# Kernel optimization log

Measured on AMD Instinct MI355X. Metric: run time of the kernel, lower is better.

## Reference

```python
import jax, jax.numpy as jnp
import numpy as np

# MoE config (matches init_kwargs)
E = 32      # num_experts
K = 4       # num_experts_per_tok (top_k)
H = 1024    # hidden_size
I = 512     # moe_intermediate_size (shared expert uses I * num_shared_experts = I)
B, S = 2, 2048
T = B * S
C = 1024
ROUTED_SCALE = 1.0


def _silu_and_mul(gu):
    g, u = jnp.split(gu, 2, axis=-1)
    return jax.nn.silu(g) * u


def setup_inputs() -> dict:
    key = jax.random.key(0)
    ks = jax.random.split(key, 6)
    s = 0.02
    return {
        "hidden_states": jax.random.normal(ks[0], (B, S, H), jnp.float32),
        "gate_w": jax.random.normal(ks[1], (E, H), jnp.float32) * s,
        "w_gate_up": jax.random.normal(ks[2], (E, H, 2 * I), jnp.float32) * s,
        "w_down": jax.random.normal(ks[3], (E, I, H), jnp.float32) * s,
        "shared_w_gate_up": jax.random.normal(ks[4], (H, 2 * I), jnp.float32) * s,
        "shared_w_down": jax.random.normal(ks[5], (I, H), jnp.float32) * s,
    }


def reference(hidden_states, gate_w, w_gate_up, w_down, shared_w_gate_up, shared_w_down):
    b, s, h = hidden_states.shape
    x = hidden_states.reshape(-1, h)                      # [T, H]
    t = x.shape[0]

    # --- router: gate linear -> softmax -> top-k -> renormalize ---
    logits = x @ gate_w.T                                 # [T, E]
    probs = jax.nn.softmax(logits, axis=-1)
    topk_w, topk_idx = jax.lax.top_k(probs, K)            # [T, K]
    topk_w = topk_w / jnp.sum(topk_w, axis=-1, keepdims=True)  # norm_topk_prob
    topk_w = topk_w * ROUTED_SCALE

    # --- dispatch: sort (token, slot) assignments by expert, scatter into capacity buffer ---
    e_flat = topk_idx.reshape(-1)                         # [T*K]
    w_flat = topk_w.reshape(-1)
    t_flat = jnp.repeat(jnp.arange(t), K)
    order = jnp.argsort(e_flat)                           # stable sort by expert id
    e_s, w_s, t_s = e_flat[order], w_flat[order], t_flat[order]
    counts = jax.ops.segment_sum(jnp.ones_like(e_s), e_s, num_segments=E)
    starts = jnp.cumsum(counts) - counts                  # exclusive prefix sum
    pos = jnp.arange(t * K) - starts[e_s]                 # position within expert group
    slot = jnp.minimum(pos, C)                            # overflow -> trash slot C
    buf = jnp.zeros((E, C + 1, h), x.dtype).at[e_s, slot].set(x[t_s])

    # --- grouped expert MLP (silu-gated) ---
    gu = jnp.einsum('ech,ehi->eci', buf[:, :C], w_gate_up)        # [E, C, 2I]
    expert_out = jnp.einsum('eci,eih->ech', _silu_and_mul(gu), w_down)  # [E, C, H]
    expert_out = jnp.pad(expert_out, ((0, 0), (0, 1), (0, 0)))    # trash slot reads zero

    # --- combine: gather back, weight, scatter-add per token ---
    gate = jnp.where(pos < C, w_s, 0.0)[:, None]
    routed = jnp.zeros_like(x).at[t_s].add(expert_out[e_s, slot] * gate)

    # --- shared expert MLP ---
    shared = _silu_and_mul(x @ shared_w_gate_up) @ shared_w_down

    return (routed + shared).reshape(b, s, h)
```

## Files before the change

kernel.cpp:

```cpp
#include <hip/hip_runtime.h>
#include <cstdint>
#include <cstddef>

#define NEXP   32
#define TOPK   4
#define HD     1024
#define ID     512
#define TT     4096
#define CAP    1024
#define SHARED_BASE (NEXP*CAP)
#define NSLOT  (NEXP*CAP + TT)
#define MAXTILES 320

#define KSPLIT 16
#define KCH    64
#define KSUB   16

typedef __attribute__((ext_vector_type(4))) float f32x4;
typedef __bf16 bf16x8 __attribute__((ext_vector_type(8)));

__device__ __forceinline__ unsigned short f2bf(float f) {
    union { float f; unsigned int u; } v; v.f = f;
    unsigned int u = v.u;
    u = (u + 0x7FFFu + ((u >> 16) & 1u)) >> 16;
    return (unsigned short)u;
}
__device__ __forceinline__ float bf2f(unsigned short s) {
    union { unsigned int u; float f; } v; v.u = ((unsigned int)s) << 16;
    return v.f;
}

#define GLOAD_LDS16(g, l)                                                     \
    __builtin_amdgcn_global_load_lds(                                         \
        (__attribute__((address_space(1))) void*)(g),                         \
        (__attribute__((address_space(3))) void*)(l), 16, 0, 0)

__global__ __launch_bounds__(256)
void k_prep(const float* __restrict__ wgu, const float* __restrict__ sgu,
            const float* __restrict__ wdn, const float* __restrict__ sdn,
            unsigned short* __restrict__ wgup_t, unsigned short* __restrict__ wdn_t,
            const float* __restrict__ x, const float* __restrict__ gw,
            float* __restrict__ part, unsigned short* __restrict__ xb) {
    __shared__ __align__(16) char smem[18944];
    const int z = blockIdx.z;
    const int tid = threadIdx.x;

    if (z < 66) {
        const float* src; const float* srcS; unsigned short* dst; int K, N, zz;
        if (z < 33) { src = wgu; srcS = sgu; dst = wgup_t; K = 1024; N = 1024; zz = z; }
        else {
            if (blockIdx.y >= 8) return;
            src = wdn; srcS = sdn; dst = wdn_t; K = 512; N = 1024; zz = z - 33;
        }
        float (*ld)[65] = reinterpret_cast<float(*)[65]>(smem);
        const size_t esz = (size_t)K * N;
        const float* s = (zz < NEXP) ? src + (size_t)zz * esz : srcS;
        dst += (size_t)zz * esz;
        const int n0 = blockIdx.x * 64, k0 = blockIdx.y * 64;
        const int c4 = (tid & 15) * 4;
        const int rbase = tid >> 4;
#pragma unroll
        for (int p = 0; p < 4; p++) {
            int row = rbase + p * 16;
            float4 v = *(const float4*)(s + (size_t)(k0 + row) * N + n0 + c4);
            ld[row][c4 + 0] = v.x; ld[row][c4 + 1] = v.y;
            ld[row][c4 + 2] = v.z; ld[row][c4 + 3] = v.w;
        }
        __syncthreads();
        const int n  = tid >> 2;
        const int ks = (tid & 3) * 16;
        unsigned short tmp[16];
#pragma unroll
        for (int i = 0; i < 16; i++) tmp[i] = f2bf(ld[ks + i][n]);
        uint4 a, b;
        a.x = tmp[0] | (tmp[1] << 16);  a.y = tmp[2] | (tmp[3] << 16);
        a.z = tmp[4] | (tmp[5] << 16);  a.w = tmp[6] | (tmp[7] << 16);
        b.x = tmp[8] | (tmp[9] << 16);  b.y = tmp[10] | (tmp[11] << 16);
        b.z = tmp[12] | (tmp[13] << 16); b.w = tmp[14] | (tmp[15] << 16);
        unsigned short* op = dst + (size_t)(n0 + n) * K + k0 + ks;
        *(uint4*)op = a;
        *(uint4*)(op + 8) = b;
        return;
    }

    float (*xsT)[260] = reinterpret_cast<float(*)[260]>(smem);
    float (*gsT)[36]  = reinterpret_cast<float(*)[36]>(smem + KSUB * 260 * 4);
    const int lane = tid & 63, wv = tid >> 6;
    const int tg = lane >> 2, eg = lane & 3;
    const int t0 = blockIdx.x * 256;
    const int kbase = blockIdx.y * KCH;
    const int tbase = wv * 64 + tg * 4;
    const int ebase = eg * 8;

    float acc[4][8];
#pragma unroll
    for (int j = 0; j < 4; j++)
#pragma unroll
        for (int i = 0; i < 8; i++) acc[j][i] = 0.f;

    for (int ks = 0; ks < KCH; ks += KSUB) {
        const int k0 = kbase + ks;
        if (ks > 0) __syncthreads();
#pragma unroll
        for (int p = 0; p < 4; p++) {
            int vid = p * 256 + tid;
            int t = vid >> 2, kq = (vid & 3) * 4;
            float4 v = *(const float4*)(x + (size_t)(t0 + t) * HD + k0 + kq);
            xsT[kq + 0][t] = v.x; xsT[kq + 1][t] = v.y;
            xsT[kq + 2][t] = v.z; xsT[kq + 3][t] = v.w;
            ushort4 o;
            o.x = f2bf(v.x); o.y = f2bf(v.y); o.z = f2bf(v.z); o.w = f2bf(v.w);
            *(ushort4*)(xb + (size_t)(t0 + t) * HD + k0 + kq) = o;
        }
#pragma unroll
        for (int p = 0; p < 2; p++) {
            int vid = p * 256 + tid;
            int e = vid >> 4, k = vid & 15;
            gsT[k][e] = gw[(size_t)e * HD + k0 + k];
        }
        __syncthreads();
#pragma unroll 4
        for (int k = 0; k < KSUB; k++) {
            float4 xv = *(const float4*)&xsT[k][tbase];
            float4 g0 = *(const float4*)&gsT[k][ebase];
            float4 g1 = *(const float4*)&gsT[k][ebase + 4];
            float xa[4] = {xv.x, xv.y, xv.z, xv.w};
#pragma unroll
            for (int j = 0; j < 4; j++) {
                acc[j][0] += xa[j] * g0.x; acc[j][1] += xa[j] * g0.y;
                acc[j][2] += xa[j] * g0.z; acc[j][3] += xa[j] * g0.w;
                acc[j][4] += xa[j] * g1.x; acc[j][5] += xa[j] * g1.y;
                acc[j][6] += xa[j] * g1.z; acc[j][7] += xa[j] * g1.w;
            }
        }
    }
    const size_t base = ((size_t)blockIdx.y * TT + (t0 + tbase)) * 32 + ebase;
#pragma unroll
    for (int j = 0; j < 4; j++) {
        float4 w0, w1;
        w0.x = acc[j][0]; w0.y = acc[j][1]; w0.z = acc[j][2]; w0.w = acc[j][3];
        w1.x = acc[j][4]; w1.y = acc[j][5]; w1.z = acc[j][6]; w1.w = acc[j][7];
        *(float4*)(part + base + (size_t)j * 32) = w0;
        *(float4*)(part + base + (size_t)j * 32 + 4) = w1;
    }
}

__global__ __launch_bounds__(256)
void k_topk(const float* __restrict__ part,
            int* __restrict__ choice, float* __restrict__ cw,
            int* __restrict__ tok, float* __restrict__ wgt) {
    const int lane = threadIdx.x & 63, wv = threadIdx.x >> 6;
    const int t = blockIdx.x * 4 + wv;
    const int e = lane & 31;
    const int sbase = (lane >> 5) * 8;
    float v = 0.f;
#pragma unroll
    for (int s = 0; s < 8; s++)
        v += part[((size_t)(sbase + s) * TT + t) * 32 + e];
    v += __shfl_xor(v, 32);
    float sc = (lane < 32) ? v : -INFINITY;

    float lv[TOPK]; int le[TOPK];
#pragma unroll
    for (int r = 0; r < TOPK; r++) {
        float m = sc;
#pragma unroll
        for (int d = 1; d < 64; d <<= 1) m = fmaxf(m, __shfl_xor(m, d));
        unsigned long long ball = __ballot(sc == m);
        int widx = __ffsll(ball) - 1;
        lv[r] = m; le[r] = widx;
        if (lane == widx) sc = -INFINITY;
    }
    if (lane == 0) {
        float wv4[TOPK], wsum = 0.f;
#pragma unroll
        for (int r = 0; r < TOPK; r++) { wv4[r] = __expf(lv[r] - lv[0]); wsum += wv4[r]; }
#pragma unroll
        for (int r = 0; r < TOPK; r++) {
            choice[t * TOPK + r] = le[r];
            cw[t * TOPK + r] = wv4[r] / wsum;
        }
        tok[SHARED_BASE + t] = t;
        wgt[SHARED_BASE + t] = 1.0f;
    }
}

__global__ __launch_bounds__(1024)
void k_assign(const int* __restrict__ choice, const float* __restrict__ cw,
              int* __restrict__ cnt, int* __restrict__ tok,
              float* __restrict__ wgt, int* __restrict__ smap) {
    const int e = blockIdx.x;
    const int tid = threadIdx.x, lane = tid & 63, wv = tid >> 6;
    __shared__ int wtot[16];
    int running = 0;
    for (int it = 0; it < TT / 1024; it++) {
        const int t = it * 1024 + tid;
        const int4   c4 = *(const int4*)(choice + t * 4);
        const float4 w4 = *(const float4*)(cw + t * 4);
        unsigned m = (unsigned)(c4.x == e) | ((unsigned)(c4.y == e) << 1)
                   | ((unsigned)(c4.z == e) << 2) | ((unsigned)(c4.w == e) << 3);
        int mc = __popc(m);
        int pre = mc;
#pragma unroll
        for (int d = 1; d < 64; d <<= 1) {
            int up = __shfl_up(pre, d);
            if (lane >= d) pre += up;
        }
        if (lane == 63) wtot[wv] = pre;
        const int wpre = pre - mc;
        __syncthreads();
        int woff = 0, tot = 0;
#pragma unroll
        for (int w = 0; w < 16; w++) { int c = wtot[w]; tot += c; if (w < wv) woff += c; }
        int base = running + woff + wpre;
        running += tot;
        __syncthreads();
        if (m) {
            const float wa[4] = {w4.x, w4.y, w4.z, w4.w};
            int k = 0;
#pragma unroll
            for (int r = 0; r < 4; r++) {
                if (m & (1u << r)) {
                    int pos = base + k;
                    int i = t * 4 + r;
                    if (pos < CAP) {
                        int slot = e * CAP + pos;
                        tok[slot] = t;
                        wgt[slot] = wa[r];
                        smap[i] = slot;
                    } else {
                        smap[i] = -1;
                    }
                    k++;
                }
            }
        }
    }
    if (tid == 0) cnt[e] = min(running, CAP);
}

template <int KD, bool GATHER, bool SILU>
__global__ __launch_bounds__(256)
void k_moe_gemm(const unsigned short* __restrict__ Ab,
                const unsigned short* __restrict__ Bt,
                unsigned short* __restrict__ Cout,
                const int* __restrict__ tok,
                const int* __restrict__ cnt) {
    const int tid  = threadIdx.x;
    const int lane = tid & 63;
    const int wv   = tid >> 6;

    int c_l = (lane < NEXP) ? min(cnt[lane], CAP) : ((lane == NEXP) ? TT : 0);
    int nt_l = (c_l + 127) >> 7;
    int pre = nt_l;
#pragma unroll
    for (int d = 1; d < 64; d <<= 1) {
        int up = __shfl_up(pre, d);
        if (lane >= d) pre += up;
    }
    const int ntl = __shfl(pre, 63);
    const int chunk = (ntl + 7) >> 3;
    const int c_xcd = blockIdx.x;
    const int qy = blockIdx.y;
    if ((qy >> 3) >= chunk) return;
    const int j = c_xcd * chunk + (qy >> 3);
    if (j >= ntl) return;
    const int nt = qy & 7;
    const int start_l = pre - nt_l;
    const bool mine = (j >= start_l) && (j < start_l + nt_l);
    const unsigned long long bl = __ballot(mine);
    const int e_lane = __ffsll((long long)bl) - 1;
    const int e  = e_lane;
    const int mt = j - __shfl(start_l, e_lane);
    const int cE = __shfl(c_l, e_lane);

    const int slotbase = (e < NEXP) ? e * CAP : SHARED_BASE;
    const int m0 = mt * 128;
    const int rowsv = min(128, cE - m0);

    const unsigned short* Bte = Bt + (size_t)e * (1024 * KD);

    __shared__ unsigned short As[3][128 * 32];
    __shared__ unsigned short Bs[3][128 * 32];

    const int rr  = lane >> 2;
    const int seg = (lane & 3) ^ ((lane >> 3) & 3);
    const int r0 = wv * 32 + rr;
    const int r1 = r0 + 16;

    int ga0 = m0 + r0, ga1 = m0 + r1;
    int ra0, ra1;
    if (GATHER) {
        ra0 = (ga0 < cE) ? tok[slotbase + ga0] : 0;
        ra1 = (ga1 < cE) ? tok[slotbase + ga1] : 0;
    } else {
        ra0 = slotbase + ga0;
        ra1 = slotbase + ga1;
    }
    const unsigned short* ap0 = Ab + (size_t)ra0 * KD + seg * 8;
    const unsigned short* ap1 = Ab + (size_t)ra1 * KD + seg * 8;

    int br0, br1;
    if (SILU) {
        int in0 = r0 & 63, in1 = r1 & 63;
        int c0 = nt * 64 + (r0 >> 6) * 32 + (in0 & 31);
        int c1 = nt * 64 + (r1 >> 6) * 32 + (in1 & 31);
        br0 = (in0 < 32) ? c0 : 512 + c0;
        br1 = (in1 < 32) ? c1 : 512 + c1;
    } else {
        br0 = nt * 128 + r0;
        br1 = nt * 128 + r1;
    }
    const unsigned short* bp0 = Bte + (size_t)br0 * KD + seg * 8;
    const unsigned short* bp1 = Bte + (size_t)br1 * KD + seg * 8;

    const int aoff0 = (wv * 32) * 32, aoff1 = (wv * 32 + 16) * 32;

    f32x4 acc[4][4];
#pragma unroll
    for (int i = 0; i < 4; i++)
#pragma unroll
        for (int j2 = 0; j2 < 4; j2++) acc[i][j2] = (f32x4)(0.0f);

    const int mrow = lane & 15;
    const int quad = lane >> 4;
    const int wm = wv >> 1, wn = wv & 1;
    const int sw = (quad ^ ((mrow >> 1) & 3)) * 8;

    const int aRdOff = (wm * 64 + mrow) * 32 + sw;
    const int bRdOff = (wn * 64 + mrow) * 32 + sw;

    GLOAD_LDS16(ap0, As[0] + aoff0);
    GLOAD_LDS16(ap1, As[0] + aoff1);
    GLOAD_LDS16(bp0, Bs[0] + aoff0);
    GLOAD_LDS16(bp1, Bs[0] + aoff1);
    GLOAD_LDS16(ap0 + 32, As[1] + aoff0);
    GLOAD_LDS16(ap1 + 32, As[1] + aoff1);
    GLOAD_LDS16(bp0 + 32, Bs[1] + aoff0);
    GLOAD_LDS16(bp1 + 32, Bs[1] + aoff1);

    int p = 0;
    for (int k0 = 0; k0 < KD; k0 += 32) {
        if (k0 + 32 < KD) {
            asm volatile("s_waitcnt vmcnt(4) lgkmcnt(0)" ::: "memory");
        } else {
            asm volatile("s_waitcnt vmcnt(0) lgkmcnt(0)" ::: "memory");
        }
        __builtin_amdgcn_s_barrier();
        asm volatile("" ::: "memory");

        const int kn = k0 + 64;
        if (kn < KD) {
            int pw = p + 2; if (pw >= 3) pw -= 3;
            GLOAD_LDS16(ap0 + kn, As[pw] + aoff0);
            GLOAD_LDS16(ap1 + kn, As[pw] + aoff1);
            GLOAD_LDS16(bp0 + kn, Bs[pw] + aoff0);
            GLOAD_LDS16(bp1 + kn, Bs[pw] + aoff1);
        }

        bf16x8 af[4], bf[4];
#pragma unroll
        for (int i = 0; i < 4; i++) {
            af[i] = *(const bf16x8*)(As[p] + aRdOff + i * 16 * 32);
            bf[i] = *(const bf16x8*)(Bs[p] + bRdOff + i * 16 * 32);
        }
#pragma unroll
        for (int mi = 0; mi < 4; mi++)
#pragma unroll
            for (int nj = 0; nj < 4; nj++)
                acc[mi][nj] = __builtin_amdgcn_mfma_f32_16x16x32_bf16(
                    af[mi], bf[nj], acc[mi][nj], 0, 0, 0);
        p++; if (p >= 3) p = 0;
    }

    if (SILU) {
#pragma unroll
        for (int mi = 0; mi < 4; mi++)
#pragma unroll
            for (int nj = 0; nj < 2; nj++) {
                f32x4 g = acc[mi][nj];
                f32x4 u = acc[mi][nj + 2];
#pragma unroll
                for (int r = 0; r < 4; r++) {
                    int rloc = wm * 64 + mi * 16 + quad * 4 + r;
                    if (rloc < rowsv) {
                        float gv = g[r], uv = u[r];
                        float a = (gv / (1.f + __expf(-gv))) * uv;
                        int c = nt * 64 + wn * 32 + nj * 16 + mrow;
                        Cout[(size_t)(slotbase + m0 + rloc) * ID + c] = f2bf(a);
                    }
                }
            }
    } else {
#pragma unroll
        for (int mi = 0; mi < 4; mi++)
#pragma unroll
            for (int nj = 0; nj < 4; nj++) {
                f32x4 v = acc[mi][nj];
#pragma unroll
                for (int r = 0; r < 4; r++) {
                    int rloc = wm * 64 + mi * 16 + quad * 4 + r;
                    if (rloc < rowsv) {
                        int c = nt * 128 + wn * 64 + nj * 16 + mrow;
                        Cout[(size_t)(slotbase + m0 + rloc) * HD + c] = f2bf(v[r]);
                    }
                }
            }
    }
}

__global__ __launch_bounds__(256)
void k_combine(const unsigned short* __restrict__ eout,
               const int* __restrict__ smap,
               const float* __restrict__ wgt,
               float* __restrict__ out) {
    const int t = blockIdx.x;
    const int h0 = threadIdx.x * 4;
    ushort4 q = *(const ushort4*)(eout + (size_t)(SHARED_BASE + t) * HD + h0);
    float a0 = bf2f(q.x), a1 = bf2f(q.y), a2 = bf2f(q.z), a3 = bf2f(q.w);
#pragma unroll
    for (int r = 0; r < TOPK; r++) {
        int slot = smap[t * TOPK + r];
        if (slot >= 0) {
            float w = wgt[slot];
            ushort4 e4 = *(const ushort4*)(eout + (size_t)slot * HD + h0);
            a0 += w * bf2f(e4.x); a1 += w * bf2f(e4.y);
            a2 += w * bf2f(e4.z); a3 += w * bf2f(e4.w);
        }
    }
    float4 o; o.x = a0; o.y = a1; o.z = a2; o.w = a3;
    *(float4*)(out + (size_t)t * HD + h0) = o;
}

extern "C" void kernel_launch(void* const* d_in, const int* in_sizes, int n_in,
                              void* d_out, int out_size, void* d_ws, size_t ws_size,
                              hipStream_t stream) {
    const float* x   = (const float*)d_in[0];
    const float* gw  = (const float*)d_in[1];
    const float* wgu = (const float*)d_in[2];
    const float* wdn = (const float*)d_in[3];
    const float* sgu = (const float*)d_in[4];
    const float* sdn = (const float*)d_in[5];
    float* out = (float*)d_out;

    char* w = (char*)d_ws;
    size_t off = 0;
    int* cnt = (int*)(w + off);                       off += 256;
    unsigned short* xb     = (unsigned short*)(w + off); off += (size_t)TT * HD * 2;
    unsigned short* wgup_t = (unsigned short*)(w + off); off += (size_t)33 * 1024 * 1024 * 2;
    unsigned short* wdn_t  = (unsigned short*)(w + off); off += (size_t)33 * 1024 * 512 * 2;
    unsigned short* act    = (unsigned short*)(w + off); off += (size_t)NSLOT * ID * 2;
    int*   tok    = (int*)(w + off);   off += (size_t)NSLOT * 4;
    float* wgt    = (float*)(w + off); off += (size_t)NSLOT * 4;
    int*   smap   = (int*)(w + off);   off += (size_t)TT * TOPK * 4;
    int*   choice = (int*)(w + off);   off += (size_t)TT * TOPK * 4;
    float* cw     = (float*)(w + off); off += (size_t)TT * TOPK * 4;

    float* part = (float*)act;
    unsigned short* eout = xb;

    k_prep<<<dim3(16, 16, 67), 256, 0, stream>>>(wgu, sgu, wdn, sdn,
                                                 wgup_t, wdn_t, x, gw, part, xb);
    k_topk<<<TT / 4, 256, 0, stream>>>(part, choice, cw, tok, wgt);
    k_assign<<<NEXP, 1024, 0, stream>>>(choice, cw, cnt, tok, wgt, smap);

    k_moe_gemm<1024, true, true><<<dim3(8, MAXTILES), 256, 0, stream>>>(xb, wgup_t, act, tok, cnt);
    k_moe_gemm<512, false, false><<<dim3(8, MAXTILES), 256, 0, stream>>>(act, wdn_t, eout, tok, cnt);

    k_combine<<<TT, 256, 0, stream>>>(eout, smap, wgt, out);
}
```

Measured before the change: 417.5 us.

## Pipeline weight transpose-convert with async LDS loads and fewer router K-splits

```diff
diff --git a/kernel.cpp b/kernel.cpp
--- a/kernel.cpp
+++ b/kernel.cpp
@@ -12,8 +12,8 @@
 #define NSLOT  (NEXP*CAP + TT)
 #define MAXTILES 320
 
-#define KSPLIT 16
-#define KCH    64
+#define KSPLIT 4
+#define KCH    256
 #define KSUB   16
 
 typedef __attribute__((ext_vector_type(4))) float f32x4;
@@ -41,46 +41,74 @@
             unsigned short* __restrict__ wgup_t, unsigned short* __restrict__ wdn_t,
             const float* __restrict__ x, const float* __restrict__ gw,
             float* __restrict__ part, unsigned short* __restrict__ xb) {
-    __shared__ __align__(16) char smem[18944];
+    __shared__ __align__(16) char smem[49152];
     const int z = blockIdx.z;
     const int tid = threadIdx.x;
 
     if (z < 66) {
-        const float* src; const float* srcS; unsigned short* dst; int K, N, zz;
-        if (z < 33) { src = wgu; srcS = sgu; dst = wgup_t; K = 1024; N = 1024; zz = z; }
+        const float* src; const float* srcS; unsigned short* dst; int K, zz;
+        if (z < 33) { src = wgu; srcS = sgu; dst = wgup_t; K = 1024; zz = z; }
         else {
-            if (blockIdx.y >= 8) return;
-            src = wdn; srcS = sdn; dst = wdn_t; K = 512; N = 1024; zz = z - 33;
-        }
-        float (*ld)[65] = reinterpret_cast<float(*)[65]>(smem);
+            if (blockIdx.y >= 2) return;
+            src = wdn; srcS = sdn; dst = wdn_t; K = 512; zz = z - 33;
+        }
+        const int N = 1024;
+        float* ring = reinterpret_cast<float*>(smem);
         const size_t esz = (size_t)K * N;
         const float* s = (zz < NEXP) ? src + (size_t)zz * esz : srcS;
         dst += (size_t)zz * esz;
-        const int n0 = blockIdx.x * 64, k0 = blockIdx.y * 64;
-        const int c4 = (tid & 15) * 4;
-        const int rbase = tid >> 4;
-#pragma unroll
-        for (int p = 0; p < 4; p++) {
-            int row = rbase + p * 16;
-            float4 v = *(const float4*)(s + (size_t)(k0 + row) * N + n0 + c4);
-            ld[row][c4 + 0] = v.x; ld[row][c4 + 1] = v.y;
-            ld[row][c4 + 2] = v.z; ld[row][c4 + 3] = v.w;
-        }
-        __syncthreads();
+        const int n0 = blockIdx.x * 64;
+        const int kb = blockIdx.y * 256;
+        const int lane = tid & 63, wv2 = tid >> 6;
+        const int sig_w = (0x5140 >> (wv2 * 4)) & 7;
+        const int pp = (lane & 15) ^ sig_w;
+
+#define TSTAGE(ss, b)                                                         \
+        {                                                                     \
+            _Pragma("unroll")                                                 \
+            for (int q = 0; q < 4; q++) {                                     \
+                int rl = wv2 * 16 + q * 4 + (lane >> 4);                      \
+                const float* gp = s + (size_t)(kb + (ss) * 64 + rl) * N       \
+                                    + n0 + pp * 4;                            \
+                GLOAD_LDS16(gp, ring + (b) * 4096 + (wv2 * 16 + q * 4) * 64); \
+            }                                                                 \
+        }
         const int n  = tid >> 2;
         const int ks = (tid & 3) * 16;
-        unsigned short tmp[16];
-#pragma unroll
-        for (int i = 0; i < 16; i++) tmp[i] = f2bf(ld[ks + i][n]);
-        uint4 a, b;
-        a.x = tmp[0] | (tmp[1] << 16);  a.y = tmp[2] | (tmp[3] << 16);
-        a.z = tmp[4] | (tmp[5] << 16);  a.w = tmp[6] | (tmp[7] << 16);
-        b.x = tmp[8] | (tmp[9] << 16);  b.y = tmp[10] | (tmp[11] << 16);
-        b.z = tmp[12] | (tmp[13] << 16); b.w = tmp[14] | (tmp[15] << 16);
-        unsigned short* op = dst + (size_t)(n0 + n) * K + k0 + ks;
-        *(uint4*)op = a;
-        *(uint4*)(op + 8) = b;
+        const int sig_r = (0x5140 >> ((tid & 3) * 4)) & 7;
+        const int slot = (n >> 2) ^ sig_r;
+#define TPROC(ss, b)                                                          \
+        {                                                                     \
+            const float* rbp = ring + (b) * 4096 + ks * 64 + slot * 4 + (n & 3); \
+            unsigned short tmp[16];                                           \
+            _Pragma("unroll")                                                 \
+            for (int i = 0; i < 16; i++) tmp[i] = f2bf(rbp[i * 64]);          \
+            uint4 a, bq;                                                      \
+            a.x = tmp[0] | (tmp[1] << 16);  a.y = tmp[2] | (tmp[3] << 16);    \
+            a.z = tmp[4] | (tmp[5] << 16);  a.w = tmp[6] | (tmp[7] << 16);    \
+            bq.x = tmp[8] | (tmp[9] << 16);  bq.y = tmp[10] | (tmp[11] << 16);\
+            bq.z = tmp[12] | (tmp[13] << 16); bq.w = tmp[14] | (tmp[15] << 16);\
+            unsigned short* op = dst + (size_t)(n0 + n) * K + kb + (ss) * 64 + ks; \
+            *(uint4*)op = a;                                                  \
+            *(uint4*)(op + 8) = bq;                                           \
+        }
+
+        TSTAGE(0, 0); TSTAGE(1, 1);
+        asm volatile("s_waitcnt vmcnt(4)" ::: "memory");
+        __builtin_amdgcn_s_barrier();
+        TSTAGE(2, 2); TPROC(0, 0);
+        asm volatile("s_waitcnt vmcnt(6)" ::: "memory");
+        __builtin_amdgcn_s_barrier();
+        TSTAGE(3, 0); TPROC(1, 1);
+        asm volatile("s_waitcnt vmcnt(8)" ::: "memory");
+        __builtin_amdgcn_s_barrier();
+        TPROC(2, 2);
+        asm volatile("s_waitcnt vmcnt(4)" ::: "memory");
+        __builtin_amdgcn_s_barrier();
+        TPROC(3, 0);
         return;
+#undef TSTAGE
+#undef TPROC
     }
 
     float (*xsT)[260] = reinterpret_cast<float(*)[260]>(smem);
@@ -152,10 +180,10 @@
     const int lane = threadIdx.x & 63, wv = threadIdx.x >> 6;
     const int t = blockIdx.x * 4 + wv;
     const int e = lane & 31;
-    const int sbase = (lane >> 5) * 8;
+    const int sbase = (lane >> 5) * 2;
     float v = 0.f;
 #pragma unroll
-    for (int s = 0; s < 8; s++)
+    for (int s = 0; s < 2; s++)
         v += part[((size_t)(sbase + s) * TT + t) * 32 + e];
     v += __shfl_xor(v, 32);
     float sc = (lane < 32) ? v : -INFINITY;
@@ -459,8 +487,8 @@
     float* part = (float*)act;
     unsigned short* eout = xb;
 
-    k_prep<<<dim3(16, 16, 67), 256, 0, stream>>>(wgu, sgu, wdn, sdn,
-                                                 wgup_t, wdn_t, x, gw, part, xb);
+    k_prep<<<dim3(16, 4, 67), 256, 0, stream>>>(wgu, sgu, wdn, sdn,
+                                                wgup_t, wdn_t, x, gw, part, xb);
     k_topk<<<TT / 4, 256, 0, stream>>>(part, choice, cw, tok, wgt);
     k_assign<<<NEXP, 1024, 0, stream>>>(choice, cw, cnt, tok, wgt, smap);
 
```

Measured after the change: 429.0 us. 1.03x slower.

## Double-buffer weight transpose in prep kernel, processing four K-chunks per block

Applied to the files above, without the earlier changes.

```diff
diff --git a/kernel.cpp b/kernel.cpp
--- a/kernel.cpp
+++ b/kernel.cpp
@@ -12,8 +12,8 @@
 #define NSLOT  (NEXP*CAP + TT)
 #define MAXTILES 320
 
-#define KSPLIT 16
-#define KCH    64
+#define KSPLIT 4
+#define KCH    256
 #define KSUB   16
 
 typedef __attribute__((ext_vector_type(4))) float f32x4;
@@ -41,45 +41,70 @@
             unsigned short* __restrict__ wgup_t, unsigned short* __restrict__ wdn_t,
             const float* __restrict__ x, const float* __restrict__ gw,
             float* __restrict__ part, unsigned short* __restrict__ xb) {
-    __shared__ __align__(16) char smem[18944];
+    __shared__ __align__(16) char smem[33280];
     const int z = blockIdx.z;
     const int tid = threadIdx.x;
 
     if (z < 66) {
-        const float* src; const float* srcS; unsigned short* dst; int K, N, zz;
-        if (z < 33) { src = wgu; srcS = sgu; dst = wgup_t; K = 1024; N = 1024; zz = z; }
+        const float* src; const float* srcS; unsigned short* dst; int K, zz;
+        if (z < 33) { src = wgu; srcS = sgu; dst = wgup_t; K = 1024; zz = z; }
         else {
-            if (blockIdx.y >= 8) return;
-            src = wdn; srcS = sdn; dst = wdn_t; K = 512; N = 1024; zz = z - 33;
-        }
-        float (*ld)[65] = reinterpret_cast<float(*)[65]>(smem);
+            if (blockIdx.y >= 2) return;
+            src = wdn; srcS = sdn; dst = wdn_t; K = 512; zz = z - 33;
+        }
+        const int N = 1024;
+        float (*ld)[64][65] = reinterpret_cast<float(*)[64][65]>(smem);
         const size_t esz = (size_t)K * N;
         const float* s = (zz < NEXP) ? src + (size_t)zz * esz : srcS;
         dst += (size_t)zz * esz;
-        const int n0 = blockIdx.x * 64, k0 = blockIdx.y * 64;
+        const int n0 = blockIdx.x * 64;
+        const int kb = blockIdx.y * 256;
         const int c4 = (tid & 15) * 4;
         const int rbase = tid >> 4;
+        const int n  = tid >> 2;
+        const int ks = (tid & 3) * 16;
+
+        float4 rg[4];
+#pragma unroll
+        for (int p = 0; p < 4; p++)
+            rg[p] = *(const float4*)(s + (size_t)(kb + rbase + p * 16) * N + n0 + c4);
 #pragma unroll
         for (int p = 0; p < 4; p++) {
             int row = rbase + p * 16;
-            float4 v = *(const float4*)(s + (size_t)(k0 + row) * N + n0 + c4);
-            ld[row][c4 + 0] = v.x; ld[row][c4 + 1] = v.y;
-            ld[row][c4 + 2] = v.z; ld[row][c4 + 3] = v.w;
-        }
-        __syncthreads();
-        const int n  = tid >> 2;
-        const int ks = (tid & 3) * 16;
-        unsigned short tmp[16];
-#pragma unroll
-        for (int i = 0; i < 16; i++) tmp[i] = f2bf(ld[ks + i][n]);
-        uint4 a, b;
-        a.x = tmp[0] | (tmp[1] << 16);  a.y = tmp[2] | (tmp[3] << 16);
-        a.z = tmp[4] | (tmp[5] << 16);  a.w = tmp[6] | (tmp[7] << 16);
-        b.x = tmp[8] | (tmp[9] << 16);  b.y = tmp[10] | (tmp[11] << 16);
-        b.z = tmp[12] | (tmp[13] << 16); b.w = tmp[14] | (tmp[15] << 16);
-        unsigned short* op = dst + (size_t)(n0 + n) * K + k0 + ks;
-        *(uint4*)op = a;
-        *(uint4*)(op + 8) = b;
+            ld[0][row][c4 + 0] = rg[p].x; ld[0][row][c4 + 1] = rg[p].y;
+            ld[0][row][c4 + 2] = rg[p].z; ld[0][row][c4 + 3] = rg[p].w;
+        }
+
+#pragma unroll
+        for (int sIt = 0; sIt < 4; sIt++) {
+            const int cur = sIt & 1;
+            float4 rg2[4];
+            if (sIt < 3) {
+#pragma unroll
+                for (int p = 0; p < 4; p++)
+                    rg2[p] = *(const float4*)(s + (size_t)(kb + (sIt + 1) * 64 + rbase + p * 16) * N + n0 + c4);
+            }
+            __syncthreads();
+            unsigned short tmp[16];
+#pragma unroll
+            for (int i = 0; i < 16; i++) tmp[i] = f2bf(ld[cur][ks + i][n]);
+            uint4 a, bq;
+            a.x = tmp[0] | (tmp[1] << 16);  a.y = tmp[2] | (tmp[3] << 16);
+            a.z = tmp[4] | (tmp[5] << 16);  a.w = tmp[6] | (tmp[7] << 16);
+            bq.x = tmp[8] | (tmp[9] << 16);  bq.y = tmp[10] | (tmp[11] << 16);
+            bq.z = tmp[12] | (tmp[13] << 16); bq.w = tmp[14] | (tmp[15] << 16);
+            unsigned short* op = dst + (size_t)(n0 + n) * K + kb + sIt * 64 + ks;
+            *(uint4*)op = a;
+            *(uint4*)(op + 8) = bq;
+            if (sIt < 3) {
+#pragma unroll
+                for (int p = 0; p < 4; p++) {
+                    int row = rbase + p * 16;
+                    ld[cur ^ 1][row][c4 + 0] = rg2[p].x; ld[cur ^ 1][row][c4 + 1] = rg2[p].y;
+                    ld[cur ^ 1][row][c4 + 2] = rg2[p].z; ld[cur ^ 1][row][c4 + 3] = rg2[p].w;
+                }
+            }
+        }
         return;
     }
 
@@ -152,10 +177,10 @@
     const int lane = threadIdx.x & 63, wv = threadIdx.x >> 6;
     const int t = blockIdx.x * 4 + wv;
     const int e = lane & 31;
-    const int sbase = (lane >> 5) * 8;
+    const int sbase = (lane >> 5) * 2;
     float v = 0.f;
 #pragma unroll
-    for (int s = 0; s < 8; s++)
+    for (int s = 0; s < 2; s++)
         v += part[((size_t)(sbase + s) * TT + t) * 32 + e];
     v += __shfl_xor(v, 32);
     float sc = (lane < 32) ? v : -INFINITY;
@@ -459,8 +484,8 @@
     float* part = (float*)act;
     unsigned short* eout = xb;
 
-    k_prep<<<dim3(16, 16, 67), 256, 0, stream>>>(wgu, sgu, wdn, sdn,
-                                                 wgup_t, wdn_t, x, gw, part, xb);
+    k_prep<<<dim3(16, 4, 67), 256, 0, stream>>>(wgu, sgu, wdn, sdn,
+                                                wgup_t, wdn_t, x, gw, part, xb);
     k_topk<<<TT / 4, 256, 0, stream>>>(part, choice, cw, tok, wgt);
     k_assign<<<NEXP, 1024, 0, stream>>>(choice, cw, cnt, tok, wgt, smap);
 
```

Measured after the change: 427.7 us. 1.02x slower.

## Drop weight transpose in prep; transpose B tiles in-register into LDS inside GEMM

Applied to the files above, without the earlier changes.

```diff
diff --git a/kernel.cpp b/kernel.cpp
--- a/kernel.cpp
+++ b/kernel.cpp
@@ -38,7 +38,7 @@
 __global__ __launch_bounds__(256)
 void k_prep(const float* __restrict__ wgu, const float* __restrict__ sgu,
             const float* __restrict__ wdn, const float* __restrict__ sdn,
-            unsigned short* __restrict__ wgup_t, unsigned short* __restrict__ wdn_t,
+            unsigned short* __restrict__ wgup_b, unsigned short* __restrict__ wdn_b,
             const float* __restrict__ x, const float* __restrict__ gw,
             float* __restrict__ part, unsigned short* __restrict__ xb) {
     __shared__ __align__(16) char smem[18944];
@@ -46,40 +46,26 @@
     const int tid = threadIdx.x;
 
     if (z < 66) {
-        const float* src; const float* srcS; unsigned short* dst; int K, N, zz;
-        if (z < 33) { src = wgu; srcS = sgu; dst = wgup_t; K = 1024; N = 1024; zz = z; }
-        else {
-            if (blockIdx.y >= 8) return;
-            src = wdn; srcS = sdn; dst = wdn_t; K = 512; N = 1024; zz = z - 33;
-        }
-        float (*ld)[65] = reinterpret_cast<float(*)[65]>(smem);
-        const size_t esz = (size_t)K * N;
-        const float* s = (zz < NEXP) ? src + (size_t)zz * esz : srcS;
-        dst += (size_t)zz * esz;
-        const int n0 = blockIdx.x * 64, k0 = blockIdx.y * 64;
-        const int c4 = (tid & 15) * 4;
-        const int rbase = tid >> 4;
-#pragma unroll
-        for (int p = 0; p < 4; p++) {
-            int row = rbase + p * 16;
-            float4 v = *(const float4*)(s + (size_t)(k0 + row) * N + n0 + c4);
-            ld[row][c4 + 0] = v.x; ld[row][c4 + 1] = v.y;
-            ld[row][c4 + 2] = v.z; ld[row][c4 + 3] = v.w;
-        }
-        __syncthreads();
-        const int n  = tid >> 2;
-        const int ks = (tid & 3) * 16;
-        unsigned short tmp[16];
-#pragma unroll
-        for (int i = 0; i < 16; i++) tmp[i] = f2bf(ld[ks + i][n]);
-        uint4 a, b;
-        a.x = tmp[0] | (tmp[1] << 16);  a.y = tmp[2] | (tmp[3] << 16);
-        a.z = tmp[4] | (tmp[5] << 16);  a.w = tmp[6] | (tmp[7] << 16);
-        b.x = tmp[8] | (tmp[9] << 16);  b.y = tmp[10] | (tmp[11] << 16);
-        b.z = tmp[12] | (tmp[13] << 16); b.w = tmp[14] | (tmp[15] << 16);
-        unsigned short* op = dst + (size_t)(n0 + n) * K + k0 + ks;
-        *(uint4*)op = a;
-        *(uint4*)(op + 8) = b;
+        const float* s; unsigned short* d;
+        const int lb = blockIdx.y * 16 + blockIdx.x;
+        if (z < 33) {
+            s = (z < NEXP) ? wgu + (size_t)z * (1024 * 1024) : sgu;
+            d = wgup_b + (size_t)z * (1024 * 1024);
+        } else {
+            if (lb >= 128) return;
+            int zz = z - 33;
+            s = (zz < NEXP) ? wdn + (size_t)zz * (512 * 1024) : sdn;
+            d = wdn_b + (size_t)zz * (512 * 1024);
+        }
+        const size_t base = (size_t)lb * 1024;
+#pragma unroll
+        for (int j = 0; j < 4; j++) {
+            size_t i = base + j * 256 + tid;
+            float4 v = ((const float4*)s)[i];
+            ushort4 o;
+            o.x = f2bf(v.x); o.y = f2bf(v.y); o.z = f2bf(v.z); o.w = f2bf(v.w);
+            ((ushort4*)d)[i] = o;
+        }
         return;
     }
 
@@ -278,13 +264,13 @@
     const int m0 = mt * 128;
     const int rowsv = min(128, cE - m0);
 
-    const unsigned short* Bte = Bt + (size_t)e * (1024 * KD);
+    const unsigned short* Bte = Bt + (size_t)e * ((size_t)KD * 1024);
 
     __shared__ unsigned short As[3][128 * 32];
-    __shared__ unsigned short Bs[3][128 * 32];
-
-    const int rr  = lane >> 2;
-    const int seg = (lane & 3) ^ ((lane >> 3) & 3);
+    __shared__ unsigned short Bs[2][128 * 32];
+
+    const int rr   = lane >> 2;
+    const int segA = (lane & 3) ^ ((lane >> 4) & 3);
     const int r0 = wv * 32 + rr;
     const int r1 = r0 + 16;
 
@@ -297,24 +283,57 @@
         ra0 = slotbase + ga0;
         ra1 = slotbase + ga1;
     }
-    const unsigned short* ap0 = Ab + (size_t)ra0 * KD + seg * 8;
-    const unsigned short* ap1 = Ab + (size_t)ra1 * KD + seg * 8;
-
-    int br0, br1;
+    const unsigned short* ap0 = Ab + (size_t)ra0 * KD + segA * 8;
+    const unsigned short* ap1 = Ab + (size_t)ra1 * KD + segA * 8;
+    const int aoff0 = (wv * 32) * 32, aoff1 = (wv * 32 + 16) * 32;
+
+    const int hB = lane >> 5;
+    const int nw = lane & 31;
+    int rB[4], offB[4];
+    int bcol;
     if (SILU) {
-        int in0 = r0 & 63, in1 = r1 & 63;
-        int c0 = nt * 64 + (r0 >> 6) * 32 + (in0 & 31);
-        int c1 = nt * 64 + (r1 >> 6) * 32 + (in1 & 31);
-        br0 = (in0 < 32) ? c0 : 512 + c0;
-        br1 = (in1 < 32) ? c1 : 512 + c1;
+        const int sn0 = nw * 4;
+        const int side = sn0 >> 6;
+        const int jj0 = sn0 & 63;
+        bcol = (side ? 512 : 0) + nt * 64 + jj0;
+#pragma unroll
+        for (int q = 0; q < 4; q++) {
+            int jj = jj0 + q;
+            rB[q] = ((jj >> 5) << 6) + (side << 5) + (jj & 31);
+        }
     } else {
-        br0 = nt * 128 + r0;
-        br1 = nt * 128 + r1;
-    }
-    const unsigned short* bp0 = Bte + (size_t)br0 * KD + seg * 8;
-    const unsigned short* bp1 = Bte + (size_t)br1 * KD + seg * 8;
-
-    const int aoff0 = (wv * 32) * 32, aoff1 = (wv * 32 + 16) * 32;
+        bcol = nt * 128 + nw * 4;
+#pragma unroll
+        for (int q = 0; q < 4; q++) rB[q] = nw * 4 + q;
+    }
+#pragma unroll
+    for (int q = 0; q < 4; q++) {
+        int slot = wv ^ ((rB[q] >> 2) & 3);
+        offB[q] = rB[q] * 32 + slot * 8 + hB * 4;
+    }
+    const unsigned short* bp = Bte + (size_t)(wv * 8 + hB * 4) * 1024 + bcol;
+
+#define BLOAD(IT, R0, R1, R2, R3)                                             \
+    {                                                                         \
+        const unsigned short* bpk = bp + (size_t)(IT) * 32 * 1024;            \
+        R0 = *(const uint2*)(bpk);                                            \
+        R1 = *(const uint2*)(bpk + 1024);                                     \
+        R2 = *(const uint2*)(bpk + 2048);                                     \
+        R3 = *(const uint2*)(bpk + 3072);                                     \
+    }
+#define BPACK(BUF, R0, R1, R2, R3)                                            \
+    {                                                                         \
+        unsigned short* bw = &Bs[BUF][0];                                     \
+        _Pragma("unroll")                                                     \
+        for (int q = 0; q < 4; q++) {                                         \
+            unsigned e0 = ((q < 2 ? R0.x : R0.y) >> (16 * (q & 1))) & 0xffffu;\
+            unsigned e1 = ((q < 2 ? R1.x : R1.y) >> (16 * (q & 1))) & 0xffffu;\
+            unsigned e2 = ((q < 2 ? R2.x : R2.y) >> (16 * (q & 1))) & 0xffffu;\
+            unsigned e3 = ((q < 2 ? R3.x : R3.y) >> (16 * (q & 1))) & 0xffffu;\
+            uint2 wv2; wv2.x = e0 | (e1 << 16); wv2.y = e2 | (e3 << 16);      \
+            *(uint2*)(bw + offB[q]) = wv2;                                    \
+        }                                                                     \
+    }
 
     f32x4 acc[4][4];
 #pragma unroll
@@ -325,44 +344,44 @@
     const int mrow = lane & 15;
     const int quad = lane >> 4;
     const int wm = wv >> 1, wn = wv & 1;
-    const int sw = (quad ^ ((mrow >> 1) & 3)) * 8;
+    const int sw = (quad ^ ((mrow >> 2) & 3)) * 8;
 
     const int aRdOff = (wm * 64 + mrow) * 32 + sw;
     const int bRdOff = (wn * 64 + mrow) * 32 + sw;
 
+    uint2 rb0, rb1, rb2, rb3;
+    BLOAD(0, rb0, rb1, rb2, rb3);
+    __builtin_amdgcn_sched_barrier(0);
     GLOAD_LDS16(ap0, As[0] + aoff0);
     GLOAD_LDS16(ap1, As[0] + aoff1);
-    GLOAD_LDS16(bp0, Bs[0] + aoff0);
-    GLOAD_LDS16(bp1, Bs[0] + aoff1);
     GLOAD_LDS16(ap0 + 32, As[1] + aoff0);
     GLOAD_LDS16(ap1 + 32, As[1] + aoff1);
-    GLOAD_LDS16(bp0 + 32, Bs[1] + aoff0);
-    GLOAD_LDS16(bp1 + 32, Bs[1] + aoff1);
-
-    int p = 0;
-    for (int k0 = 0; k0 < KD; k0 += 32) {
-        if (k0 + 32 < KD) {
-            asm volatile("s_waitcnt vmcnt(4) lgkmcnt(0)" ::: "memory");
-        } else {
-            asm volatile("s_waitcnt vmcnt(0) lgkmcnt(0)" ::: "memory");
-        }
+    __builtin_amdgcn_sched_barrier(0);
+    BPACK(0, rb0, rb1, rb2, rb3);
+
+    const int NIT = KD / 32;
+    int pA = 0, pB = 0;
+    for (int it = 0; it < NIT; ++it) {
+        asm volatile("s_waitcnt vmcnt(2) lgkmcnt(0)" ::: "memory");
         __builtin_amdgcn_s_barrier();
         asm volatile("" ::: "memory");
 
-        const int kn = k0 + 64;
-        if (kn < KD) {
-            int pw = p + 2; if (pw >= 3) pw -= 3;
-            GLOAD_LDS16(ap0 + kn, As[pw] + aoff0);
-            GLOAD_LDS16(ap1 + kn, As[pw] + aoff1);
-            GLOAD_LDS16(bp0 + kn, Bs[pw] + aoff0);
-            GLOAD_LDS16(bp1 + kn, Bs[pw] + aoff1);
-        }
+        const bool hasB = (it + 1) < NIT;
+        const bool hasA = (it + 2) < NIT;
+        if (hasB) BLOAD(it + 1, rb0, rb1, rb2, rb3);
+        __builtin_amdgcn_sched_barrier(0);
+        if (hasA) {
+            int pw = pA + 2; if (pw >= 3) pw -= 3;
+            GLOAD_LDS16(ap0 + (it + 2) * 32, As[pw] + aoff0);
+            GLOAD_LDS16(ap1 + (it + 2) * 32, As[pw] + aoff1);
+        }
+        __builtin_amdgcn_sched_barrier(0);
 
         bf16x8 af[4], bf[4];
 #pragma unroll
         for (int i = 0; i < 4; i++) {
-            af[i] = *(const bf16x8*)(As[p] + aRdOff + i * 16 * 32);
-            bf[i] = *(const bf16x8*)(Bs[p] + bRdOff + i * 16 * 32);
+            af[i] = *(const bf16x8*)(As[pA] + aRdOff + i * 16 * 32);
+            bf[i] = *(const bf16x8*)(Bs[pB] + bRdOff + i * 16 * 32);
         }
 #pragma unroll
         for (int mi = 0; mi < 4; mi++)
@@ -370,8 +389,14 @@
             for (int nj = 0; nj < 4; nj++)
                 acc[mi][nj] = __builtin_amdgcn_mfma_f32_16x16x32_bf16(
                     af[mi], bf[nj], acc[mi][nj], 0, 0, 0);
-        p++; if (p >= 3) p = 0;
-    }
+        __builtin_amdgcn_sched_barrier(0);
+        if (hasB) BPACK(pB ^ 1, rb0, rb1, rb2, rb3);
+
+        pA++; if (pA >= 3) pA = 0;
+        pB ^= 1;
+    }
+#undef BLOAD
+#undef BPACK
 
     if (SILU) {
 #pragma unroll
@@ -447,8 +472,8 @@
     size_t off = 0;
     int* cnt = (int*)(w + off);                       off += 256;
     unsigned short* xb     = (unsigned short*)(w + off); off += (size_t)TT * HD * 2;
-    unsigned short* wgup_t = (unsigned short*)(w + off); off += (size_t)33 * 1024 * 1024 * 2;
-    unsigned short* wdn_t  = (unsigned short*)(w + off); off += (size_t)33 * 1024 * 512 * 2;
+    unsigned short* wgup_b = (unsigned short*)(w + off); off += (size_t)33 * 1024 * 1024 * 2;
+    unsigned short* wdn_b  = (unsigned short*)(w + off); off += (size_t)33 * 512 * 1024 * 2;
     unsigned short* act    = (unsigned short*)(w + off); off += (size_t)NSLOT * ID * 2;
     int*   tok    = (int*)(w + off);   off += (size_t)NSLOT * 4;
     float* wgt    = (float*)(w + off); off += (size_t)NSLOT * 4;
@@ -460,12 +485,12 @@
     unsigned short* eout = xb;
 
     k_prep<<<dim3(16, 16, 67), 256, 0, stream>>>(wgu, sgu, wdn, sdn,
-                                                 wgup_t, wdn_t, x, gw, part, xb);
+                                                 wgup_b, wdn_b, x, gw, part, xb);
     k_topk<<<TT / 4, 256, 0, stream>>>(part, choice, cw, tok, wgt);
     k_assign<<<NEXP, 1024, 0, stream>>>(choice, cw, cnt, tok, wgt, smap);
 
-    k_moe_gemm<1024, true, true><<<dim3(8, MAXTILES), 256, 0, stream>>>(xb, wgup_t, act, tok, cnt);
-    k_moe_gemm<512, false, false><<<dim3(8, MAXTILES), 256, 0, stream>>>(act, wdn_t, eout, tok, cnt);
+    k_moe_gemm<1024, true, true><<<dim3(8, MAXTILES), 256, 0, stream>>>(xb, wgup_b, act, tok, cnt);
+    k_moe_gemm<512, false, false><<<dim3(8, MAXTILES), 256, 0, stream>>>(act, wdn_b, eout, tok, cnt);
 
     k_combine<<<TT, 256, 0, stream>>>(eout, smap, wgt, out);
 }
```

After: 440.7 us. 5.5% more time.
